# Kernel tuning notes

Measured on AMD Instinct MI355X. Metric: run time of the kernel, lower is better.

The kernel has to match this reference:

```python
import jax, jax.numpy as jnp
import numpy as np
from jax import lax

NEG_INF = -1e30

def _binarize(w):
    # BinaryConnect / XNOR-style sign binarization with straight-through estimator
    return w + lax.stop_gradient(jnp.sign(w) - w)

def _conv(x, w, b):
    y = lax.conv_general_dilated(x, w, window_strides=(1, 1), padding='VALID',
                                 dimension_numbers=('NCHW', 'OIHW', 'NCHW'))
    return y + b[None, :, None, None]

def _bn(x, eps, gamma=None, beta=None):
    # training-mode batch norm over (N, H, W)
    mean = jnp.mean(x, axis=(0, 2, 3), keepdims=True)
    var = jnp.var(x, axis=(0, 2, 3), keepdims=True)
    xn = (x - mean) * lax.rsqrt(var + eps)
    if gamma is not None:
        g = jnp.clip(gamma, 0.01, None)  # torch forward clamps BN weight to >=0.01
        xn = xn * g[None, :, None, None] + beta[None, :, None, None]
    return xn

def _maxpool2(x):
    return lax.reduce_window(x, NEG_INF, lax.max, (1, 1, 2, 2), (1, 1, 2, 2), 'VALID')


def setup_inputs() -> dict:
    key = jax.random.key(0)
    ks = jax.random.split(key, 12)
    f = jnp.float32
    return {
        'x': jax.random.normal(ks[0], (8192, 1, 32, 32), dtype=f),
        'conv1_w': jax.random.normal(ks[1], (6, 1, 5, 5), dtype=f) * 0.2,
        'conv1_b': jnp.zeros((6,), dtype=f),
        'conv2_w': jax.random.normal(ks[2], (16, 6, 5, 5), dtype=f) * 0.1,
        'conv2_b': jnp.zeros((16,), dtype=f),
        'bn2_g': jnp.ones((16,), dtype=f),
        'bn2_b': jnp.zeros((16,), dtype=f),
        'conv3_w': jax.random.normal(ks[3], (120, 16, 5, 5), dtype=f) * 0.05,
        'conv3_b': jnp.zeros((120,), dtype=f),
        'bn3_g': jnp.ones((120,), dtype=f),
        'bn3_b': jnp.zeros((120,), dtype=f),
        'fc1_w': jax.random.normal(ks[4], (84, 120), dtype=f) * 0.09,
        'fc1_b': jnp.zeros((84,), dtype=f),
        'fc2_w': jax.random.normal(ks[5], (10, 84), dtype=f) * 0.1,
        'fc2_b': jnp.zeros((10,), dtype=f),
    }


def reference(x, conv1_w, conv1_b, conv2_w, conv2_b, bn2_g, bn2_b,
              conv3_w, conv3_b, bn3_g, bn3_b, fc1_w, fc1_b, fc2_w, fc2_b):
    # layer1: fp conv -> BN(no affine, eps=1e-4) -> relu -> maxpool  [B,6,14,14]
    h = _maxpool2(jax.nn.relu(_bn(_conv(x, conv1_w, conv1_b), 1e-4)))
    # layer2: binary conv -> BN(affine, eps=1e-4) -> relu -> maxpool [B,16,5,5]
    h = _maxpool2(jax.nn.relu(_bn(_conv(h, _binarize(conv2_w), conv2_b), 1e-4, bn2_g, bn2_b)))
    # layer3: binary conv -> BN(affine, eps=1e-5) -> relu            [B,120,1,1]
    h = jax.nn.relu(_bn(_conv(h, _binarize(conv3_w), conv3_b), 1e-5, bn3_g, bn3_b))
    # layer4: binary linear -> relu -> linear                        [B,10]
    h = h.reshape(h.shape[0], -1)  # [B,120]
    h = jax.nn.relu(h @ _binarize(fc1_w).T + fc1_b)
    return h @ fc2_w.T + fc2_b
```

## Files before the change

kernel.cpp:

```cpp
#include <hip/hip_runtime.h>

#define DEVFN __device__ __forceinline__

DEVFN float sgnf(float x) { return (x > 0.f) ? 1.f : ((x < 0.f) ? -1.f : 0.f); }

DEVFN unsigned short f2bf(float x) {
  unsigned int u = __float_as_uint(x);
  unsigned int r = (u + 0x7fffu + ((u >> 16) & 1u)) >> 16;
  return (unsigned short)r;
}

typedef __attribute__((ext_vector_type(8))) short short8;
typedef __attribute__((ext_vector_type(4))) float f32x4;

#define SUM1 0
#define SQ1  384
#define SUM2 768
#define SQ2  1792
#define SUM3 2816
#define SQ3  10496
#define DBL_BYTES 145408

#define A1 0
#define C1 8
#define A2 16
#define C2 32
#define A3 48
#define C3 168
#define W2B_OFF  512
#define WFR_OFF  3584
#define WFR2_OFF 54784
#define H1_OFF   69632
#define H2_OFF   (H1_OFF + 8192*1176)
#define Y3_OFF   (H2_OFF + 8192*400)

__global__ __launch_bounds__(256, 3) void conv1_prep(
    const float* __restrict__ x, const float* __restrict__ w1,
    const float* __restrict__ b1, float* __restrict__ m1,
    double* __restrict__ sums, const float* __restrict__ w2,
    const float* __restrict__ w3, const float* __restrict__ f1,
    float* __restrict__ w2t, unsigned short* __restrict__ wfr,
    unsigned short* __restrict__ wfr2) {
  __shared__ float simg[8 * 1088];
  __shared__ float swtp[6 * 40];
  __shared__ float red[6], redq[6];
  int tid = threadIdx.x;
  if (blockIdx.x >= 1024) {
    int i = (blockIdx.x - 1024) * 256 + tid;
    if (i < 2400) {
      int ci = i / 400, r = i - ci * 400;
      int k = r >> 4, ch = r & 15;
      w2t[i] = sgnf(w2[(ch * 6 + ci) * 25 + k]);
    }
    if (i < 102400) {
      int j = i & 7;
      int t = i >> 3;
      int l = t & 63;
      int cc = (t >> 6) % 25;
      int nt = (t >> 6) / 25;
      int ch = nt * 16 + (l & 15);
      int kp = cc * 32 + ((l >> 4) << 3) + j;
      float v = (ch < 120) ? sgnf(w3[ch * 400 + (kp >> 1)]) : 0.f;
      wfr[i] = f2bf(v);
    }
    if (i < 24576) {
      int j = i & 7;
      int t = i >> 3;
      int l = t & 63;
      int cc = (t >> 6) & 7;
      int nt = t >> 9;
      int col = nt * 16 + (l & 15);
      int kp = cc * 32 + ((l >> 4) << 3) + j;
      int k = kp >> 1;
      float v = (col < 84 && k < 120) ? sgnf(f1[col * 120 + k]) : 0.f;
      wfr2[i] = f2bf(v);
    }
    return;
  }
  int img0 = blockIdx.x * 8;
  {
    const float2* xg = (const float2*)(x + (size_t)img0 * 1024);
    for (int i2 = tid; i2 < 4096; i2 += 256) {
      int img = i2 >> 9;
      int r = (i2 >> 4) & 31;
      int c2 = i2 & 15;
      *(float2*)&simg[img * 1088 + r * 34 + c2 * 2] = xg[i2];
    }
  }
  for (int i = tid; i < 240; i += 256) {
    int ch = i / 40, k = i - ch * 40;
    swtp[i] = (k < 25) ? w1[ch * 25 + k] : 0.f;
  }
  if (tid < 6) { red[tid] = 0.f; redq[tid] = 0.f; }
  __syncthreads();

  for (int idx = tid; idx < 672; idx += 256) {
    int img = idx / 84;
    int r = idx - img * 84;
    int ch = r / 14;
    int py = r - ch * 14;
    float wr[25];
    {
      const float4* wp = (const float4*)&swtp[ch * 40];
#pragma unroll
      for (int t = 0; t < 6; ++t) {
        float4 v = wp[t];
        wr[4 * t] = v.x; wr[4 * t + 1] = v.y; wr[4 * t + 2] = v.z; wr[4 * t + 3] = v.w;
      }
      wr[24] = swtp[ch * 40 + 24];
    }
    float bb = b1[ch];
    float acc0[28], acc1[28];
#pragma unroll
    for (int o = 0; o < 28; ++o) { acc0[o] = bb; acc1[o] = bb; }
#pragma unroll
    for (int d = 0; d < 6; ++d) {
      int row = 2 * py + d;
      float rb[32];
      const float2* rp = (const float2*)&simg[img * 1088 + row * 34];
#pragma unroll
      for (int t = 0; t < 16; ++t) { float2 v = rp[t]; rb[2 * t] = v.x; rb[2 * t + 1] = v.y; }
      if (d < 5) {
#pragma unroll
        for (int kx = 0; kx < 5; ++kx) {
          float w = wr[d * 5 + kx];
#pragma unroll
          for (int o = 0; o < 28; ++o) acc0[o] = fmaf(rb[o + kx], w, acc0[o]);
        }
      }
      if (d >= 1) {
#pragma unroll
        for (int kx = 0; kx < 5; ++kx) {
          float w = wr[(d - 1) * 5 + kx];
#pragma unroll
          for (int o = 0; o < 28; ++o) acc1[o] = fmaf(rb[o + kx], w, acc1[o]);
        }
      }
    }
    float s = 0.f, s2 = 0.f;
#pragma unroll
    for (int o = 0; o < 28; ++o) {
      s += acc0[o] + acc1[o];
      s2 = fmaf(acc0[o], acc0[o], s2);
      s2 = fmaf(acc1[o], acc1[o], s2);
    }
    atomicAdd(&red[ch], s);
    atomicAdd(&redq[ch], s2);
    float* mp = m1 + (size_t)(img0 + img) * 1176 + ch * 196 + py * 14;
#pragma unroll
    for (int j = 0; j < 7; ++j) {
      float2 v;
      v.x = fmaxf(fmaxf(acc0[4 * j], acc0[4 * j + 1]), fmaxf(acc1[4 * j], acc1[4 * j + 1]));
      v.y = fmaxf(fmaxf(acc0[4 * j + 2], acc0[4 * j + 3]), fmaxf(acc1[4 * j + 2], acc1[4 * j + 3]));
      *(float2*)&mp[2 * j] = v;
    }
  }
  __syncthreads();
  if (tid < 6) {
    int slot = blockIdx.x & 63;
    atomicAdd(&sums[SUM1 + tid * 64 + slot], (double)red[tid]);
    atomicAdd(&sums[SQ1 + tid * 64 + slot], (double)redq[tid]);
  }
}

__global__ __launch_bounds__(256) void finalize_bn(
    const double* __restrict__ sum, const double* __restrict__ sq, int nch,
    double invN, double eps, const float* __restrict__ gamma,
    const float* __restrict__ beta, float* __restrict__ a,
    float* __restrict__ c) {
  int t = blockIdx.x * 256 + threadIdx.x;
  int ch = t >> 6, slot = t & 63;
  if (ch >= nch) return;
  double s = sum[ch * 64 + slot];
  double q = sq[ch * 64 + slot];
#pragma unroll
  for (int off = 32; off > 0; off >>= 1) {
    s += __shfl_down(s, off, 64);
    q += __shfl_down(q, off, 64);
  }
  if (slot == 0) {
    double mean = s * invN;
    double var = q * invN - mean * mean;
    float inv = (float)(1.0 / sqrt(var + eps));
    float g = gamma ? fmaxf(gamma[ch], 0.01f) : 1.f;
    float av = g * inv;
    float cv = (beta ? beta[ch] : 0.f) - (float)mean * av;
    a[ch] = av;
    c[ch] = cv;
  }
}

__global__ __launch_bounds__(320, 5) void conv2_fused(
    const float* __restrict__ m1, const float* __restrict__ w2t,
    const float* __restrict__ b2, const float* __restrict__ scales,
    float* __restrict__ m2, double* __restrict__ sums) {
  __shared__ float sh1[4 * 1352];
  __shared__ float swt[2400];
  __shared__ float sa1[6], sc1[6];
  __shared__ float red[16], redq[16];
  int tid = threadIdx.x;
  int img0 = blockIdx.x * 4;
  if (tid < 6) { sa1[tid] = scales[A1 + tid]; sc1[tid] = scales[C1 + tid]; }
  if (tid < 16) { red[tid] = 0.f; redq[tid] = 0.f; }
  __syncthreads();
  {
    const float4* wg = (const float4*)w2t;
    float4* w4 = (float4*)swt;
    for (int i4 = tid; i4 < 600; i4 += 320) w4[i4] = wg[i4];
  }
  {
    const float2* mg = (const float2*)(m1 + (size_t)img0 * 1176);
    for (int i2 = tid; i2 < 2352; i2 += 320) {
      int img = i2 / 588;
      int r = i2 - img * 588;
      int pl = r / 98;
      int rr = r - pl * 98;
      int row = rr / 7, t = rr - row * 7;
      float a = sa1[pl], c = sc1[pl];
      float2 v = mg[i2];
      v.x = fmaxf(fmaf(a, v.x, c), 0.f);
      v.y = fmaxf(fmaf(a, v.y, c), 0.f);
      *(float2*)&sh1[img * 1352 + pl * 224 + row * 16 + t * 2] = v;
    }
  }
  __syncthreads();

  int ch = tid & 15;
  int img = (tid >> 4) & 3;
  int pr = tid >> 6;
  float bb = b2[ch];
  float acc[2][10];
#pragma unroll
  for (int o = 0; o < 10; ++o) { acc[0][o] = bb; acc[1][o] = bb; }
  const float* ibase = &sh1[img * 1352];
  for (int ci = 0; ci < 6; ++ci) {
    float w[25];
#pragma unroll
    for (int k = 0; k < 25; ++k) w[k] = swt[ci * 400 + k * 16 + ch];
    const float* rbase = ibase + ci * 224 + pr * 32;
#pragma unroll
    for (int d = 0; d < 6; ++d) {
      float rb[16];
      const float4* rp = (const float4*)(rbase + d * 16);
#pragma unroll
      for (int t = 0; t < 4; ++t) {
        float4 v = rp[t];
        rb[4 * t] = v.x; rb[4 * t + 1] = v.y; rb[4 * t + 2] = v.z; rb[4 * t + 3] = v.w;
      }
      if (d < 5) {
#pragma unroll
        for (int kx = 0; kx < 5; ++kx) {
          float wv = w[d * 5 + kx];
#pragma unroll
          for (int o = 0; o < 10; ++o) acc[0][o] = fmaf(rb[o + kx], wv, acc[0][o]);
        }
      }
      if (d >= 1) {
#pragma unroll
        for (int kx = 0; kx < 5; ++kx) {
          float wv = w[(d - 1) * 5 + kx];
#pragma unroll
          for (int o = 0; o < 10; ++o) acc[1][o] = fmaf(rb[o + kx], wv, acc[1][o]);
        }
      }
    }
  }
  float s0 = 0.f, q0 = 0.f;
#pragma unroll
  for (int rr2 = 0; rr2 < 2; ++rr2)
#pragma unroll
    for (int o = 0; o < 10; ++o) {
      float v = acc[rr2][o];
      s0 += v;
      q0 = fmaf(v, v, q0);
    }
  {
    float* mpo = m2 + (size_t)(img0 + img) * 400 + ch * 25 + pr * 5;
#pragma unroll
    for (int pc = 0; pc < 5; ++pc)
      mpo[pc] = fmaxf(fmaxf(acc[0][2 * pc], acc[0][2 * pc + 1]),
                      fmaxf(acc[1][2 * pc], acc[1][2 * pc + 1]));
  }
  s0 += __shfl_xor(s0, 16, 64); q0 += __shfl_xor(q0, 16, 64);
  s0 += __shfl_xor(s0, 32, 64); q0 += __shfl_xor(q0, 32, 64);
  if ((tid & 48) == 0) {
    atomicAdd(&red[ch], s0);
    atomicAdd(&redq[ch], q0);
  }
  __syncthreads();
  if (tid < 16) {
    int slot = blockIdx.x & 63;
    atomicAdd(&sums[SUM2 + tid * 64 + slot], (double)red[tid]);
    atomicAdd(&sums[SQ2 + tid * 64 + slot], (double)redq[tid]);
  }
}

__global__ __launch_bounds__(256) void conv3_mfma(
    const float* __restrict__ m2, const unsigned short* __restrict__ wfr,
    const float* __restrict__ b3, const float* __restrict__ scales,
    float* __restrict__ y3, double* __restrict__ sums) {
  __shared__ unsigned int Alds[16 * 404];
  __shared__ float sa2[16], sc2[16];
  __shared__ float red[128], redq[128];
  int tid = threadIdx.x;
  int img0 = blockIdx.x * 16;
  if (tid < 16) { sa2[tid] = scales[A2 + tid]; sc2[tid] = scales[C2 + tid]; }
  if (tid < 128) { red[tid] = 0.f; redq[tid] = 0.f; }
  __syncthreads();
  for (int i4 = tid; i4 < 1600; i4 += 256) {
    int img = i4 / 100, k4 = i4 - img * 100;
    int k = 4 * k4;
    float4 v = *(const float4*)(m2 + (size_t)(img0 + img) * 400 + k);
    float vv[4] = {v.x, v.y, v.z, v.w};
    unsigned int pk[4];
#pragma unroll
    for (int e = 0; e < 4; ++e) {
      int ch = ((k + e) * 41) >> 10;
      float val = fmaxf(fmaf(sa2[ch], vv[e], sc2[ch]), 0.f);
      unsigned int hb = f2bf(val);
      float vh = __uint_as_float(hb << 16);
      unsigned int lb = f2bf(val - vh);
      pk[e] = hb | (lb << 16);
    }
    unsigned int* dst = &Alds[img * 404 + k];
    dst[0] = pk[0]; dst[1] = pk[1]; dst[2] = pk[2]; dst[3] = pk[3];
  }
  __syncthreads();

  int lane = tid & 63;
  int wv = tid >> 6;
  int nt0 = wv * 2, nt1 = wv * 2 + 1;
  const short8* bvec = (const short8*)wfr;
  int arow = lane & 15;
  int ag = lane >> 4;
  f32x4 acc0 = {0.f, 0.f, 0.f, 0.f}, acc1 = {0.f, 0.f, 0.f, 0.f};
  const unsigned short* abase =
      (const unsigned short*)&Alds[arow * 404 + ag * 4];
#pragma unroll 5
  for (int c = 0; c < 25; ++c) {
    short8 af = *(const short8*)(abase + c * 32);
    short8 b0 = bvec[(nt0 * 25 + c) * 64 + lane];
    short8 b1 = bvec[(nt1 * 25 + c) * 64 + lane];
    acc0 = __builtin_amdgcn_mfma_f32_16x16x32_bf16(af, b0, acc0, 0, 0, 0);
    acc1 = __builtin_amdgcn_mfma_f32_16x16x32_bf16(af, b1, acc1, 0, 0, 0);
  }
  int chA = nt0 * 16 + (lane & 15);
  int chB = nt1 * 16 + (lane & 15);
  int rbase = img0 + ((lane >> 4) << 2);
  {
    float bias = b3[chA];
    float s = 0.f, q = 0.f;
#pragma unroll
    for (int r = 0; r < 4; ++r) {
      float v = acc0[r] + bias;
      y3[(size_t)(rbase + r) * 120 + chA] = v;
      s += v; q = fmaf(v, v, q);
    }
    atomicAdd(&red[chA], s);
    atomicAdd(&redq[chA], q);
  }
  if (chB < 120) {
    float bias = b3[chB];
    float s = 0.f, q = 0.f;
#pragma unroll
    for (int r = 0; r < 4; ++r) {
      float v = acc1[r] + bias;
      y3[(size_t)(rbase + r) * 120 + chB] = v;
      s += v; q = fmaf(v, v, q);
    }
    atomicAdd(&red[chB], s);
    atomicAdd(&redq[chB], q);
  }
  __syncthreads();
  if (tid < 120) {
    int slot = blockIdx.x & 63;
    atomicAdd(&sums[SUM3 + tid * 64 + slot], (double)red[tid]);
    atomicAdd(&sums[SQ3 + tid * 64 + slot], (double)redq[tid]);
  }
}

__global__ __launch_bounds__(192) void fc_mfma(
    const float* __restrict__ y3, const float* __restrict__ scales,
    const unsigned short* __restrict__ wfr2, const float* __restrict__ b1,
    const float* __restrict__ w2, const float* __restrict__ b2,
    float* __restrict__ out) {
  __shared__ unsigned int Alds[16 * 132];
  __shared__ float sh4[16 * 88];
  __shared__ float sw2[10 * 85];
  __shared__ float sa3[120], sc3[120];
  __shared__ float sb1[84], sb2[10];
  int tid = threadIdx.x;
  int img0 = blockIdx.x * 16;
  if (tid < 120) { sa3[tid] = scales[A3 + tid]; sc3[tid] = scales[C3 + tid]; }
  if (tid < 84) sb1[tid] = b1[tid];
  if (tid >= 84 && tid < 94) sb2[tid - 84] = b2[tid - 84];
  for (int i = tid; i < 850; i += 192) {
    int o = i / 85, k = i - o * 85;
    sw2[i] = (k < 84) ? w2[o * 84 + k] : 0.f;
  }
  __syncthreads();
  for (int i4 = tid; i4 < 512; i4 += 192) {
    int img = i4 >> 5, k4 = i4 & 31;
    int k = 4 * k4;
    unsigned int pk[4] = {0u, 0u, 0u, 0u};
    if (k4 < 30) {
      float4 v = *(const float4*)(y3 + (size_t)(img0 + img) * 120 + k);
      float vv[4] = {v.x, v.y, v.z, v.w};
#pragma unroll
      for (int e = 0; e < 4; ++e) {
        float val = fmaxf(fmaf(sa3[k + e], vv[e], sc3[k + e]), 0.f);
        unsigned int hb = f2bf(val);
        float vh = __uint_as_float(hb << 16);
        unsigned int lb = f2bf(val - vh);
        pk[e] = hb | (lb << 16);
      }
    }
    unsigned int* dst = &Alds[img * 132 + k];
    dst[0] = pk[0]; dst[1] = pk[1]; dst[2] = pk[2]; dst[3] = pk[3];
  }
  __syncthreads();

  int lane = tid & 63;
  int wv = tid >> 6;
  int nt0 = wv * 2, nt1 = wv * 2 + 1;
  const short8* bvec = (const short8*)wfr2;
  int arow = lane & 15;
  int ag = lane >> 4;
  f32x4 acc0 = {0.f, 0.f, 0.f, 0.f}, acc1 = {0.f, 0.f, 0.f, 0.f};
  const unsigned short* abase =
      (const unsigned short*)&Alds[arow * 132 + ag * 4];
#pragma unroll
  for (int c = 0; c < 8; ++c) {
    short8 af = *(const short8*)(abase + c * 32);
    short8 b0 = bvec[(nt0 * 8 + c) * 64 + lane];
    short8 b1 = bvec[(nt1 * 8 + c) * 64 + lane];
    acc0 = __builtin_amdgcn_mfma_f32_16x16x32_bf16(af, b0, acc0, 0, 0, 0);
    acc1 = __builtin_amdgcn_mfma_f32_16x16x32_bf16(af, b1, acc1, 0, 0, 0);
  }
  {
    int jA = nt0 * 16 + (lane & 15);
    int jB = nt1 * 16 + (lane & 15);
    int r0 = (lane >> 4) << 2;
#pragma unroll
    for (int r = 0; r < 4; ++r)
      sh4[(r0 + r) * 88 + jA] = fmaxf(acc0[r] + sb1[jA], 0.f);
    if (jB < 84) {
#pragma unroll
      for (int r = 0; r < 4; ++r)
        sh4[(r0 + r) * 88 + jB] = fmaxf(acc1[r] + sb1[jB], 0.f);
    }
  }
  __syncthreads();
  if (tid < 160) {
    int img = tid / 10, o = tid - (tid / 10) * 10;
    float acc = sb2[o];
    const float* hp = &sh4[img * 88];
    const float* wp = &sw2[o * 85];
#pragma unroll 4
    for (int k = 0; k < 84; ++k) acc = fmaf(hp[k], wp[k], acc);
    out[(size_t)(img0 + img) * 10 + o] = acc;
  }
}

extern "C" void kernel_launch(void* const* d_in, const int* in_sizes, int n_in,
                              void* d_out, int out_size, void* d_ws,
                              size_t ws_size, hipStream_t stream) {
  const float* x = (const float*)d_in[0];
  const float* conv1_w = (const float*)d_in[1];
  const float* conv1_b = (const float*)d_in[2];
  const float* conv2_w = (const float*)d_in[3];
  const float* conv2_b = (const float*)d_in[4];
  const float* bn2_g = (const float*)d_in[5];
  const float* bn2_b = (const float*)d_in[6];
  const float* conv3_w = (const float*)d_in[7];
  const float* conv3_b = (const float*)d_in[8];
  const float* bn3_g = (const float*)d_in[9];
  const float* bn3_b = (const float*)d_in[10];
  const float* fc1_w = (const float*)d_in[11];
  const float* fc1_b = (const float*)d_in[12];
  const float* fc2_w = (const float*)d_in[13];
  const float* fc2_b = (const float*)d_in[14];
  float* out = (float*)d_out;

  double* sums = (double*)d_ws;
  float* fbase = (float*)((char*)d_ws + DBL_BYTES);
  float* scales = fbase;
  float* w2t = fbase + W2B_OFF;
  unsigned short* wfr = (unsigned short*)(fbase + WFR_OFF);
  unsigned short* wfr2 = (unsigned short*)(fbase + WFR2_OFF);
  float* m1 = fbase + H1_OFF;
  float* m2 = fbase + H2_OFF;
  float* y3 = fbase + Y3_OFF;

  hipMemsetAsync(d_ws, 0, DBL_BYTES, stream);

  conv1_prep<<<1424, 256, 0, stream>>>(x, conv1_w, conv1_b, m1, sums, conv2_w,
                                       conv3_w, fc1_w, w2t, wfr, wfr2);
  finalize_bn<<<2, 256, 0, stream>>>(sums + SUM1, sums + SQ1, 6,
                                     1.0 / (8192.0 * 784.0), 1e-4, nullptr,
                                     nullptr, scales + A1, scales + C1);

  conv2_fused<<<2048, 320, 0, stream>>>(m1, w2t, conv2_b, scales, m2, sums);
  finalize_bn<<<4, 256, 0, stream>>>(sums + SUM2, sums + SQ2, 16,
                                     1.0 / (8192.0 * 100.0), 1e-4, bn2_g, bn2_b,
                                     scales + A2, scales + C2);

  conv3_mfma<<<512, 256, 0, stream>>>(m2, wfr, conv3_b, scales, y3, sums);
  finalize_bn<<<30, 256, 0, stream>>>(sums + SUM3, sums + SQ3, 120,
                                      1.0 / 8192.0, 1e-5, bn3_g, bn3_b,
                                      scales + A3, scales + C3);

  fc_mfma<<<512, 192, 0, stream>>>(y3, scales, wfr2, fc1_b, fc2_w, fc2_b, out);
}
```

Baseline: 219.0 us.

## Compute five conv2 output rows per thread and stage 8 images per block

conv2 now has each thread accumulate 5 conv rows instead of 2. Every loaded input row is reused across up to 5 kernel rows, which cuts redundant LDS reads (9 row loads instead of 6 per 2 rows). Blocks are regrouped to 8 images with 256 threads. The weight layout is changed to per-channel contiguous rows padded to 28, so weights load as float4. Pooling across the two thread halves uses a shared-memory handoff with an extra barrier. The 50 accumulators raise register pressure and lower occupancy.

Measured after the change: 230.9 us. 5.5% more time.

```diff
diff --git a/kernel.cpp b/kernel.cpp
--- a/kernel.cpp
+++ b/kernel.cpp
@@ -47,10 +47,10 @@
   int tid = threadIdx.x;
   if (blockIdx.x >= 1024) {
     int i = (blockIdx.x - 1024) * 256 + tid;
-    if (i < 2400) {
-      int ci = i / 400, r = i - ci * 400;
-      int k = r >> 4, ch = r & 15;
-      w2t[i] = sgnf(w2[(ch * 6 + ci) * 25 + k]);
+    if (i < 2688) {
+      int ci = i / 448, r = i - ci * 448;
+      int ch = r / 28, k = r - ch * 28;
+      w2t[i] = (k < 25) ? sgnf(w2[(ch * 6 + ci) * 25 + k]) : 0.f;
     }
     if (i < 102400) {
       int j = i & 7;
@@ -190,27 +190,27 @@
   }
 }
 
-__global__ __launch_bounds__(320, 5) void conv2_fused(
+__global__ __launch_bounds__(256, 3) void conv2_fused(
     const float* __restrict__ m1, const float* __restrict__ w2t,
     const float* __restrict__ b2, const float* __restrict__ scales,
     float* __restrict__ m2, double* __restrict__ sums) {
-  __shared__ float sh1[4 * 1352];
-  __shared__ float swt[2400];
+  __shared__ float sh1[8 * 1352];
+  __shared__ float swt[2688];
   __shared__ float sa1[6], sc1[6];
   __shared__ float red[16], redq[16];
   int tid = threadIdx.x;
-  int img0 = blockIdx.x * 4;
+  int img0 = blockIdx.x * 8;
   if (tid < 6) { sa1[tid] = scales[A1 + tid]; sc1[tid] = scales[C1 + tid]; }
   if (tid < 16) { red[tid] = 0.f; redq[tid] = 0.f; }
   __syncthreads();
   {
     const float4* wg = (const float4*)w2t;
     float4* w4 = (float4*)swt;
-    for (int i4 = tid; i4 < 600; i4 += 320) w4[i4] = wg[i4];
+    for (int i4 = tid; i4 < 672; i4 += 256) w4[i4] = wg[i4];
   }
   {
     const float2* mg = (const float2*)(m1 + (size_t)img0 * 1176);
-    for (int i2 = tid; i2 < 2352; i2 += 320) {
+    for (int i2 = tid; i2 < 4704; i2 += 256) {
       int img = i2 / 588;
       int r = i2 - img * 588;
       int pl = r / 98;
@@ -226,20 +226,29 @@
   __syncthreads();
 
   int ch = tid & 15;
-  int img = (tid >> 4) & 3;
-  int pr = tid >> 6;
+  int img = (tid >> 4) & 7;
+  int pr = tid >> 7;
   float bb = b2[ch];
-  float acc[2][10];
-#pragma unroll
-  for (int o = 0; o < 10; ++o) { acc[0][o] = bb; acc[1][o] = bb; }
-  const float* ibase = &sh1[img * 1352];
+  float acc[5][10];
+#pragma unroll
+  for (int r = 0; r < 5; ++r)
+#pragma unroll
+    for (int o = 0; o < 10; ++o) acc[r][o] = bb;
+  const float* ibase = &sh1[img * 1352 + pr * 80];
   for (int ci = 0; ci < 6; ++ci) {
     float w[25];
-#pragma unroll
-    for (int k = 0; k < 25; ++k) w[k] = swt[ci * 400 + k * 16 + ch];
-    const float* rbase = ibase + ci * 224 + pr * 32;
-#pragma unroll
-    for (int d = 0; d < 6; ++d) {
+    {
+      const float4* wp = (const float4*)&swt[ci * 448 + ch * 28];
+#pragma unroll
+      for (int t = 0; t < 6; ++t) {
+        float4 v = wp[t];
+        w[4 * t] = v.x; w[4 * t + 1] = v.y; w[4 * t + 2] = v.z; w[4 * t + 3] = v.w;
+      }
+      w[24] = swt[ci * 448 + ch * 28 + 24];
+    }
+    const float* rbase = ibase + ci * 224;
+#pragma unroll
+    for (int d = 0; d < 9; ++d) {
       float rb[16];
       const float4* rp = (const float4*)(rbase + d * 16);
 #pragma unroll
@@ -247,47 +256,62 @@
         float4 v = rp[t];
         rb[4 * t] = v.x; rb[4 * t + 1] = v.y; rb[4 * t + 2] = v.z; rb[4 * t + 3] = v.w;
       }
-      if (d < 5) {
-#pragma unroll
-        for (int kx = 0; kx < 5; ++kx) {
-          float wv = w[d * 5 + kx];
-#pragma unroll
-          for (int o = 0; o < 10; ++o) acc[0][o] = fmaf(rb[o + kx], wv, acc[0][o]);
+#pragma unroll
+      for (int ky = 0; ky < 5; ++ky) {
+        int r = d - ky;
+        if (r >= 0 && r < 5) {
+#pragma unroll
+          for (int kx = 0; kx < 5; ++kx) {
+            float wv = w[ky * 5 + kx];
+#pragma unroll
+            for (int o = 0; o < 10; ++o)
+              acc[r][o] = fmaf(rb[o + kx], wv, acc[r][o]);
+          }
         }
       }
-      if (d >= 1) {
-#pragma unroll
-        for (int kx = 0; kx < 5; ++kx) {
-          float wv = w[(d - 1) * 5 + kx];
-#pragma unroll
-          for (int o = 0; o < 10; ++o) acc[1][o] = fmaf(rb[o + kx], wv, acc[1][o]);
-        }
-      }
     }
   }
   float s0 = 0.f, q0 = 0.f;
 #pragma unroll
-  for (int rr2 = 0; rr2 < 2; ++rr2)
+  for (int r = 0; r < 5; ++r)
 #pragma unroll
     for (int o = 0; o < 10; ++o) {
-      float v = acc[rr2][o];
+      float v = acc[r][o];
       s0 += v;
       q0 = fmaf(v, v, q0);
     }
-  {
-    float* mpo = m2 + (size_t)(img0 + img) * 400 + ch * 25 + pr * 5;
-#pragma unroll
-    for (int pc = 0; pc < 5; ++pc)
-      mpo[pc] = fmaxf(fmaxf(acc[0][2 * pc], acc[0][2 * pc + 1]),
-                      fmaxf(acc[1][2 * pc], acc[1][2 * pc + 1]));
-  }
+  float xp[5][5];
+#pragma unroll
+  for (int r = 0; r < 5; ++r)
+#pragma unroll
+    for (int j = 0; j < 5; ++j)
+      xp[r][j] = fmaxf(acc[r][2 * j], acc[r][2 * j + 1]);
   s0 += __shfl_xor(s0, 16, 64); q0 += __shfl_xor(q0, 16, 64);
   s0 += __shfl_xor(s0, 32, 64); q0 += __shfl_xor(q0, 32, 64);
   if ((tid & 48) == 0) {
     atomicAdd(&red[ch], s0);
     atomicAdd(&redq[ch], q0);
   }
-  __syncthreads();
+  float* mpo = m2 + (size_t)(img0 + img) * 400 + ch * 25;
+  float* sp = swt;
+  __syncthreads();
+  if (pr == 0) {
+#pragma unroll
+    for (int j = 0; j < 5; ++j) {
+      mpo[j] = fmaxf(xp[0][j], xp[1][j]);
+      mpo[5 + j] = fmaxf(xp[2][j], xp[3][j]);
+      sp[(img * 16 + ch) * 5 + j] = xp[4][j];
+    }
+  }
+  __syncthreads();
+  if (pr == 1) {
+#pragma unroll
+    for (int j = 0; j < 5; ++j) {
+      mpo[10 + j] = fmaxf(sp[(img * 16 + ch) * 5 + j], xp[0][j]);
+      mpo[15 + j] = fmaxf(xp[1][j], xp[2][j]);
+      mpo[20 + j] = fmaxf(xp[3][j], xp[4][j]);
+    }
+  }
   if (tid < 16) {
     int slot = blockIdx.x & 63;
     atomicAdd(&sums[SUM2 + tid * 64 + slot], (double)red[tid]);
@@ -500,7 +524,7 @@
                                      1.0 / (8192.0 * 784.0), 1e-4, nullptr,
                                      nullptr, scales + A1, scales + C1);
 
-  conv2_fused<<<2048, 320, 0, stream>>>(m1, w2t, conv2_b, scales, m2, sums);
+  conv2_fused<<<1024, 256, 0, stream>>>(m1, w2t, conv2_b, scales, m2, sums);
   finalize_bn<<<4, 256, 0, stream>>>(sums + SUM2, sums + SQ2, 16,
                                      1.0 / (8192.0 * 100.0), 1e-4, bn2_g, bn2_b,
                                      scales + A2, scales + C2);
```

## Rewrite conv2 as bf16 MFMA implicit GEMM with split hi/lo activations

Applied to the files above, without the earlier changes.

Replaces the scalar FMA direct convolution for layer 2 with an implicit-GEMM kernel using 16x16x32 bf16 MFMA instructions. Binarized weights are pre-packed into MFMA fragment layout. Activations are stored in LDS as packed hi/lo bf16 pairs so the product stays close to fp32 precision. Each output row is a pooled 2x2 quad, so maxpool reduces to a max over the four accumulator lanes. This cuts ALU work in the conv2 stage, at the cost of extra packing work and a reused y3 buffer region for the weights.

Result: faster. 194.7 us (-11.1%).

```diff
diff --git a/kernel.cpp b/kernel.cpp
--- a/kernel.cpp
+++ b/kernel.cpp
@@ -12,6 +12,7 @@
 
 typedef __attribute__((ext_vector_type(8))) short short8;
 typedef __attribute__((ext_vector_type(4))) float f32x4;
+typedef __attribute__((ext_vector_type(4))) unsigned int u32x4;
 
 #define SUM1 0
 #define SQ1  384
@@ -27,19 +28,22 @@
 #define C2 32
 #define A3 48
 #define C3 168
-#define W2B_OFF  512
 #define WFR_OFF  3584
 #define WFR2_OFF 54784
 #define H1_OFF   69632
 #define H2_OFF   (H1_OFF + 8192*1176)
 #define Y3_OFF   (H2_OFF + 8192*400)
 
+#define RS 17
+#define PLANE 238
+#define IMGP 1428
+
 __global__ __launch_bounds__(256, 3) void conv1_prep(
     const float* __restrict__ x, const float* __restrict__ w1,
     const float* __restrict__ b1, float* __restrict__ m1,
     double* __restrict__ sums, const float* __restrict__ w2,
     const float* __restrict__ w3, const float* __restrict__ f1,
-    float* __restrict__ w2t, unsigned short* __restrict__ wfr,
+    unsigned short* __restrict__ wfr3, unsigned short* __restrict__ wfr,
     unsigned short* __restrict__ wfr2) {
   __shared__ float simg[8 * 1088];
   __shared__ float swtp[6 * 40];
@@ -47,10 +51,18 @@
   int tid = threadIdx.x;
   if (blockIdx.x >= 1024) {
     int i = (blockIdx.x - 1024) * 256 + tid;
-    if (i < 2400) {
-      int ci = i / 400, r = i - ci * 400;
-      int k = r >> 4, ch = r & 15;
-      w2t[i] = sgnf(w2[(ch * 6 + ci) * 25 + k]);
+    if (i < 7680) {
+      int j = i & 7;
+      int t = i >> 3;
+      int l = t & 63;
+      int c = t >> 6;
+      int ch = l & 15;
+      int kp = c * 32 + ((l >> 4) << 3) + j;
+      int k = kp >> 1;
+      int b = k >> 3, kx = k & 7;
+      int ci = b / 5, ky = b - 5 * ci;
+      float v = (kx < 5) ? sgnf(w2[(ch * 6 + ci) * 25 + ky * 5 + kx]) : 0.f;
+      wfr3[i] = f2bf(v);
     }
     if (i < 102400) {
       int j = i & 7;
@@ -190,100 +202,98 @@
   }
 }
 
-__global__ __launch_bounds__(320, 5) void conv2_fused(
-    const float* __restrict__ m1, const float* __restrict__ w2t,
+__global__ __launch_bounds__(256, 4) void conv2_mfma(
+    const float* __restrict__ m1, const unsigned short* __restrict__ wfr3,
     const float* __restrict__ b2, const float* __restrict__ scales,
     float* __restrict__ m2, double* __restrict__ sums) {
-  __shared__ float sh1[4 * 1352];
-  __shared__ float swt[2400];
+  __shared__ unsigned int Aim[4 * IMGP];
   __shared__ float sa1[6], sc1[6];
   __shared__ float red[16], redq[16];
   int tid = threadIdx.x;
   int img0 = blockIdx.x * 4;
   if (tid < 6) { sa1[tid] = scales[A1 + tid]; sc1[tid] = scales[C1 + tid]; }
   if (tid < 16) { red[tid] = 0.f; redq[tid] = 0.f; }
-  __syncthreads();
-  {
-    const float4* wg = (const float4*)w2t;
-    float4* w4 = (float4*)swt;
-    for (int i4 = tid; i4 < 600; i4 += 320) w4[i4] = wg[i4];
-  }
+  for (int i = tid; i < 1008; i += 256) {
+    int c3 = i - (i / 3) * 3;
+    int t = i / 3;
+    int row = t % 14;
+    int t2 = t / 14;
+    int ci = t2 % 6, img = t2 / 6;
+    Aim[img * IMGP + ci * PLANE + row * RS + 14 + c3] = 0u;
+  }
+  __syncthreads();
   {
     const float2* mg = (const float2*)(m1 + (size_t)img0 * 1176);
-    for (int i2 = tid; i2 < 2352; i2 += 320) {
+    for (int i2 = tid; i2 < 2352; i2 += 256) {
       int img = i2 / 588;
-      int r = i2 - img * 588;
-      int pl = r / 98;
-      int rr = r - pl * 98;
-      int row = rr / 7, t = rr - row * 7;
+      int e = (i2 - img * 588) * 2;
+      int pl = e / 196;
+      int rr = e - pl * 196;
+      int row = rr / 14, col = rr - row * 14;
       float a = sa1[pl], c = sc1[pl];
       float2 v = mg[i2];
-      v.x = fmaxf(fmaf(a, v.x, c), 0.f);
-      v.y = fmaxf(fmaf(a, v.y, c), 0.f);
-      *(float2*)&sh1[img * 1352 + pl * 224 + row * 16 + t * 2] = v;
-    }
-  }
-  __syncthreads();
-
-  int ch = tid & 15;
-  int img = (tid >> 4) & 3;
-  int pr = tid >> 6;
+      float v0 = fmaxf(fmaf(a, v.x, c), 0.f);
+      float v1 = fmaxf(fmaf(a, v.y, c), 0.f);
+      unsigned int h0 = f2bf(v0);
+      unsigned int l0 = f2bf(v0 - __uint_as_float(h0 << 16));
+      unsigned int h1 = f2bf(v1);
+      unsigned int l1 = f2bf(v1 - __uint_as_float(h1 << 16));
+      unsigned int* dst = &Aim[img * IMGP + pl * PLANE + row * RS + col];
+      dst[0] = h0 | (l0 << 16);
+      dst[1] = h1 | (l1 << 16);
+    }
+  }
+  __syncthreads();
+
+  int lane = tid & 63;
+  int wv = tid >> 6;
+  const short8* bvec = (const short8*)wfr3;
+  short8 bf[15];
+#pragma unroll
+  for (int c = 0; c < 15; ++c) bf[c] = bvec[c * 64 + lane];
+  int ch = lane & 15;
+  int ag = lane >> 4;
+  int agh = ag >> 1, agl = ag & 1;
   float bb = b2[ch];
-  float acc[2][10];
-#pragma unroll
-  for (int o = 0; o < 10; ++o) { acc[0][o] = bb; acc[1][o] = bb; }
-  const float* ibase = &sh1[img * 1352];
-  for (int ci = 0; ci < 6; ++ci) {
-    float w[25];
-#pragma unroll
-    for (int k = 0; k < 25; ++k) w[k] = swt[ci * 400 + k * 16 + ch];
-    const float* rbase = ibase + ci * 224 + pr * 32;
-#pragma unroll
-    for (int d = 0; d < 6; ++d) {
-      float rb[16];
-      const float4* rp = (const float4*)(rbase + d * 16);
-#pragma unroll
-      for (int t = 0; t < 4; ++t) {
-        float4 v = rp[t];
-        rb[4 * t] = v.x; rb[4 * t + 1] = v.y; rb[4 * t + 2] = v.z; rb[4 * t + 3] = v.w;
-      }
-      if (d < 5) {
-#pragma unroll
-        for (int kx = 0; kx < 5; ++kx) {
-          float wv = w[d * 5 + kx];
-#pragma unroll
-          for (int o = 0; o < 10; ++o) acc[0][o] = fmaf(rb[o + kx], wv, acc[0][o]);
-        }
-      }
-      if (d >= 1) {
-#pragma unroll
-        for (int kx = 0; kx < 5; ++kx) {
-          float wv = w[(d - 1) * 5 + kx];
-#pragma unroll
-          for (int o = 0; o < 10; ++o) acc[1][o] = fmaf(rb[o + kx], wv, acc[1][o]);
-        }
-      }
-    }
-  }
   float s0 = 0.f, q0 = 0.f;
-#pragma unroll
-  for (int rr2 = 0; rr2 < 2; ++rr2)
-#pragma unroll
-    for (int o = 0; o < 10; ++o) {
-      float v = acc[rr2][o];
-      s0 += v;
-      q0 = fmaf(v, v, q0);
-    }
-  {
-    float* mpo = m2 + (size_t)(img0 + img) * 400 + ch * 25 + pr * 5;
-#pragma unroll
-    for (int pc = 0; pc < 5; ++pc)
-      mpo[pc] = fmaxf(fmaxf(acc[0][2 * pc], acc[0][2 * pc + 1]),
-                      fmaxf(acc[1][2 * pc], acc[1][2 * pc + 1]));
+
+  for (int t = wv; t < 25; t += 4) {
+    int prd = t * 16 + ch;
+    int imr = prd / 100;
+    int pos = prd - imr * 100;
+    int pb = pos >> 2, q = pos & 3;
+    int pyr = pb / 5;
+    int py = 2 * pyr + (q >> 1);
+    int px = 2 * (pb - pyr * 5) + (q & 1);
+    const unsigned int* base = &Aim[imr * IMGP + py * RS + px + agl * 4];
+    const unsigned int* bR = base + agh * RS;
+    const unsigned int* bW = base + agh * 170;
+    f32x4 acc = {0.f, 0.f, 0.f, 0.f};
+#pragma unroll
+    for (int c = 0; c < 15; ++c) {
+      const int b0 = 2 * c;
+      const int ci0 = b0 / 5, ky0 = b0 % 5;
+      const unsigned int* pc =
+          ((ky0 == 4) ? bW : bR) + (ci0 * PLANE + ky0 * RS);
+      unsigned int a0 = pc[0], a1 = pc[1], a2 = pc[2], a3 = pc[3];
+      union { u32x4 u; short8 s; } ua;
+      ua.u = (u32x4){a0, a1, a2, a3};
+      acc = __builtin_amdgcn_mfma_f32_16x16x32_bf16(ua.s, bf[c], acc, 0, 0, 0);
+    }
+    int po = t * 4 + ag;
+    int imo = po / 25;
+    int pbl = po - imo * 25;
+    float v0 = acc[0] + bb, v1 = acc[1] + bb;
+    float v2 = acc[2] + bb, v3 = acc[3] + bb;
+    s0 += (v0 + v1) + (v2 + v3);
+    q0 = fmaf(v0, v0, q0); q0 = fmaf(v1, v1, q0);
+    q0 = fmaf(v2, v2, q0); q0 = fmaf(v3, v3, q0);
+    float mx = fmaxf(fmaxf(v0, v1), fmaxf(v2, v3));
+    m2[(size_t)(img0 + imo) * 400 + ch * 25 + pbl] = mx;
   }
   s0 += __shfl_xor(s0, 16, 64); q0 += __shfl_xor(q0, 16, 64);
   s0 += __shfl_xor(s0, 32, 64); q0 += __shfl_xor(q0, 32, 64);
-  if ((tid & 48) == 0) {
+  if (ag == 0) {
     atomicAdd(&red[ch], s0);
     atomicAdd(&redq[ch], q0);
   }
@@ -485,22 +495,22 @@
   double* sums = (double*)d_ws;
   float* fbase = (float*)((char*)d_ws + DBL_BYTES);
   float* scales = fbase;
-  float* w2t = fbase + W2B_OFF;
   unsigned short* wfr = (unsigned short*)(fbase + WFR_OFF);
   unsigned short* wfr2 = (unsigned short*)(fbase + WFR2_OFF);
   float* m1 = fbase + H1_OFF;
   float* m2 = fbase + H2_OFF;
   float* y3 = fbase + Y3_OFF;
+  unsigned short* wfr3 = (unsigned short*)y3;
 
   hipMemsetAsync(d_ws, 0, DBL_BYTES, stream);
 
   conv1_prep<<<1424, 256, 0, stream>>>(x, conv1_w, conv1_b, m1, sums, conv2_w,
-                                       conv3_w, fc1_w, w2t, wfr, wfr2);
+                                       conv3_w, fc1_w, wfr3, wfr, wfr2);
   finalize_bn<<<2, 256, 0, stream>>>(sums + SUM1, sums + SQ1, 6,
                                      1.0 / (8192.0 * 784.0), 1e-4, nullptr,
                                      nullptr, scales + A1, scales + C1);
 
-  conv2_fused<<<2048, 320, 0, stream>>>(m1, w2t, conv2_b, scales, m2, sums);
+  conv2_mfma<<<2048, 256, 0, stream>>>(m1, wfr3, conv2_b, scales, m2, sums);
   finalize_bn<<<4, 256, 0, stream>>>(sums + SUM2, sums + SQ2, 16,
                                      1.0 / (8192.0 * 100.0), 1e-4, bn2_g, bn2_b,
                                      scales + A2, scales + C2);
```
